# Kernel tuning notes

Measured on AMD Instinct MI355X. Metric: run time of the kernel, lower is better.

## Reference

```python
import jax, jax.numpy as jnp
import numpy as np

N = 50000      # nodes (== nbr_nodes)
E = 800000     # edges
D_IN = 128
D_H = 128
D_OUT = 47
NOISE_RATE = 0.1
EPS = 1e-12


def _lin_init(key, out_f, in_f):
    # rough Glorot-style init for a PyG Linear weight [out_f, in_f]
    s = 1.0 / np.sqrt(in_f)
    return jax.random.uniform(key, (out_f, in_f), jnp.float32, -s, s)


def setup_inputs() -> dict:
    key = jax.random.key(0)
    ks = jax.random.split(key, 13)
    inp = {
        "x": jax.random.normal(ks[0], (N, D_IN), jnp.float32),
        "edge_index": jax.random.randint(ks[1], (2, E), 0, N, dtype=jnp.int32),
        "noise": jax.random.normal(ks[2], (N, D_IN), jnp.float32),
        # layer 0: in -> hidden
        "W_l0": _lin_init(ks[3], D_H, D_IN),
        "b_l0": jnp.zeros((D_H,), jnp.float32),
        "W_r0": _lin_init(ks[4], D_H, D_IN),
        # layer 1: hidden -> hidden
        "W_l1": _lin_init(ks[5], D_H, D_H),
        "b_l1": jnp.zeros((D_H,), jnp.float32),
        "W_r1": _lin_init(ks[6], D_H, D_H),
        # layer 2: hidden -> out
        "W_l2": _lin_init(ks[7], D_OUT, D_H),
        "b_l2": jnp.zeros((D_OUT,), jnp.float32),
        "W_r2": _lin_init(ks[8], D_OUT, D_H),
    }
    return inp


def _sage_conv(x, src, dst, W_l, b_l, W_r):
    # PyG SAGEConv with mean aggregation:
    #   out_i = W_l @ mean_{j in N(i)} x_j + b_l + W_r @ x_i
    msg = x[src]                                              # [E, d] gather
    ssum = jax.ops.segment_sum(msg, dst, num_segments=N)      # [N, d]
    cnt = jax.ops.segment_sum(jnp.ones((src.shape[0], 1), x.dtype), dst,
                              num_segments=N)                 # [N, 1]
    agg = ssum / jnp.maximum(cnt, 1.0)                        # mean; 0 for isolated nodes
    return agg @ W_l.T + b_l + x @ W_r.T


def _branch(x, src, dst, params):
    # stacked SAGEConv; relu after all but last layer; dropout is identity (eval mode)
    h = None
    n_layers = len(params)
    for i, (W_l, b_l, W_r) in enumerate(params):
        x = _sage_conv(x, src, dst, W_l, b_l, W_r)
        if i != n_layers - 1:
            x = jax.nn.relu(x)
            h = x
    return h, jax.nn.log_softmax(x, axis=1), x


def _add_noise(x, noise):
    # n_id=None path: x + sign(x) * F.normalize(noise, dim=1) * noise_rate
    norm = jnp.sqrt(jnp.sum(noise * noise, axis=1, keepdims=True))
    unit = noise / jnp.maximum(norm, EPS)
    return x + jnp.sign(x) * unit * NOISE_RATE


def reference(x, edge_index, noise,
              W_l0, b_l0, W_r0, W_l1, b_l1, W_r1, W_l2, b_l2, W_r2):
    src, dst = edge_index[0], edge_index[1]
    params = [(W_l0, b_l0, W_r0), (W_l1, b_l1, W_r1), (W_l2, b_l2, W_r2)]
    h_p, y_p, z_p = _branch(x, src, dst, params)
    h_n, y_n, z_n = _branch(_add_noise(x, noise), src, dst, params)
    return (h_p, y_p, z_p, h_n, y_n, z_n)
```

## Files before the change

kernel.cpp:

```cpp
#include <hip/hip_runtime.h>
#include <math.h>


typedef unsigned int uint;
typedef unsigned short ushort;
typedef unsigned char uchar;
typedef short bf16x8 __attribute__((ext_vector_type(8)));
typedef float f32x4 __attribute__((ext_vector_type(4)));

__device__ __forceinline__ ushort f2b(float f) {
  union { float f; uint u; } v; v.f = f;
  uint u = v.u;
  return (ushort)((u + 0x7FFFu + ((u >> 16) & 1u)) >> 16);
}
__device__ __forceinline__ float b2f_lo(uint u) {
  union { uint u; float f; } v; v.u = u << 16; return v.f;
}
__device__ __forceinline__ float b2f_hi(uint u) {
  union { uint u; float f; } v; v.u = u & 0xFFFF0000u; return v.f;
}

#if __has_builtin(__builtin_amdgcn_cvt_f32_fp8)
__device__ __forceinline__ float dec8_0(uint u) { return __builtin_amdgcn_cvt_f32_fp8(u, 0); }
__device__ __forceinline__ float dec8_1(uint u) { return __builtin_amdgcn_cvt_f32_fp8(u, 1); }
__device__ __forceinline__ float dec8_2(uint u) { return __builtin_amdgcn_cvt_f32_fp8(u, 2); }
__device__ __forceinline__ float dec8_3(uint u) { return __builtin_amdgcn_cvt_f32_fp8(u, 3); }
#else
__device__ __forceinline__ float dec8_b(uint b) {
  uint s = (b >> 7) & 1u, ex = (b >> 3) & 0xFu, m = b & 7u;
  union { uint u; float f; } v;
  if (ex == 0) {
    v.f = (float)m * 0.001953125f;
    v.u |= s << 31;
    return v.f;
  }
  v.u = (s << 31) | ((ex + 120u) << 23) | (m << 20);
  return v.f;
}
__device__ __forceinline__ float dec8_0(uint u) { return dec8_b(u & 0xFFu); }
__device__ __forceinline__ float dec8_1(uint u) { return dec8_b((u >> 8) & 0xFFu); }
__device__ __forceinline__ float dec8_2(uint u) { return dec8_b((u >> 16) & 0xFFu); }
__device__ __forceinline__ float dec8_3(uint u) { return dec8_b((u >> 24) & 0xFFu); }
#endif

#if __has_builtin(__builtin_amdgcn_cvt_pk_fp8_f32)
__device__ __forceinline__ uchar enc8(float f) {
  return (uchar)(__builtin_amdgcn_cvt_pk_fp8_f32(f, f, 0u, false) & 0xFFu);
}
#else
__device__ __forceinline__ uchar enc8(float f) {
  union { float f; uint u; } v; v.f = f;
  uint s = v.u >> 31;
  uint a = v.u & 0x7FFFFFFFu;
  if (a >= 0x43E00000u) return (uchar)((s << 7) | 0x7Eu);
  if (a < 0x3C800000u) {
    float q = fabsf(f) * 512.0f;
    uint m = (uint)(q + 0.5f);
    return (uchar)((s << 7) | m);
  }
  uint r = a + 0x00080000u;
  if (r >= 0x43E00000u) return (uchar)((s << 7) | 0x7Eu);
  uint ex = (r >> 23) - 120u;
  uint m = (r >> 20) & 7u;
  return (uchar)((s << 7) | (ex << 3) | m);
}
#endif

__global__ __launch_bounds__(256) void count_kernel(
    const int* __restrict__ dst, int* __restrict__ cnt,
    int* __restrict__ rank, int E) {
  int e = blockIdx.x * blockDim.x + threadIdx.x;
  if (e >= E) return;
  rank[e] = atomicAdd(&cnt[dst[e]], 1);
}

__global__ __launch_bounds__(256) void scan_blocks(
    const int* __restrict__ cnt, int* __restrict__ loc,
    int* __restrict__ bsum, int n) {
  __shared__ int ls[4];
  int t = threadIdx.x;
  int base = blockIdx.x * 1024 + t * 4;
  int v[4];
  int s = 0;
#pragma unroll
  for (int i = 0; i < 4; ++i) {
    v[i] = (base + i < n) ? cnt[base + i] : 0;
    s += v[i];
  }
  int lane = t & 63, wid = t >> 6;
  int ps = s;
#pragma unroll
  for (int d = 1; d < 64; d <<= 1) {
    int o = __shfl_up(ps, d, 64);
    if (lane >= d) ps += o;
  }
  if (lane == 63) ls[wid] = ps;
  __syncthreads();
  if (t == 0) {
    int r = 0;
#pragma unroll
    for (int w = 0; w < 4; ++w) { int x = ls[w]; ls[w] = r; r += x; }
  }
  __syncthreads();
  int run = ps - s + ls[wid];
#pragma unroll
  for (int i = 0; i < 4; ++i) {
    if (base + i < n) loc[base + i] = run;
    run += v[i];
  }
  if (t == 255) bsum[blockIdx.x] = ps + ls[wid];
}

__global__ __launch_bounds__(256) void scan_bsums(int* __restrict__ bsum,
                                                  int nb) {
  __shared__ int ls[4];
  int t = threadIdx.x;
  int v = (t < nb) ? bsum[t] : 0;
  int lane = t & 63, wid = t >> 6;
  int ps = v;
#pragma unroll
  for (int d = 1; d < 64; d <<= 1) {
    int o = __shfl_up(ps, d, 64);
    if (lane >= d) ps += o;
  }
  if (lane == 63) ls[wid] = ps;
  __syncthreads();
  if (t == 0) {
    int r = 0;
#pragma unroll
    for (int w = 0; w < 4; ++w) { int x = ls[w]; ls[w] = r; r += x; }
  }
  __syncthreads();
  if (t < nb) bsum[t] = ps - v + ls[wid];
}

__global__ __launch_bounds__(256) void scan_apply(
    const int* __restrict__ loc, const int* __restrict__ bsum,
    int* __restrict__ off, int n, int E) {
  int i = blockIdx.x * 256 + threadIdx.x;
  if (i < n) off[i] = loc[i] + bsum[i >> 10];
  if (i == 0) off[n] = E;
}

__global__ __launch_bounds__(256) void fill_kernel(
    const int* __restrict__ src, const int* __restrict__ dst,
    const int* __restrict__ rank, const int* __restrict__ off,
    int* __restrict__ csr, int E) {
  int e = blockIdx.x * blockDim.x + threadIdx.x;
  if (e >= E) return;
  csr[off[dst[e]] + rank[e]] = src[e];
}

__global__ __launch_bounds__(256) void noisy_convert(
    const float* __restrict__ x, const float* __restrict__ noise,
    ushort* __restrict__ XB, int N) {
  int node = (blockIdx.x * blockDim.x + threadIdx.x) >> 6;
  int lane = threadIdx.x & 63;
  if (node >= N) return;
  size_t base = (size_t)node * 128 + 2 * lane;
  float2 nz = *(const float2*)(noise + base);
  float ss = nz.x * nz.x + nz.y * nz.y;
#pragma unroll
  for (int m = 1; m < 64; m <<= 1) ss += __shfl_xor(ss, m, 64);
  float scale = 0.1f / fmaxf(sqrtf(ss), 1e-12f);
  float2 xv = *(const float2*)(x + base);
  float s0 = (xv.x > 0.f) ? 1.f : ((xv.x < 0.f) ? -1.f : 0.f);
  float s1 = (xv.y > 0.f) ? 1.f : ((xv.y < 0.f) ? -1.f : 0.f);
  float n0 = xv.x + s0 * nz.x * scale;
  float n1 = xv.y + s1 * nz.y * scale;
  uint pc = ((uint)f2b(xv.y) << 16) | f2b(xv.x);
  uint pn = ((uint)f2b(n1) << 16) | f2b(n0);
  *(uint*)(XB + (size_t)(2 * node) * 128 + 2 * lane) = pc;
  *(uint*)(XB + (size_t)(2 * node + 1) * 128 + 2 * lane) = pn;
}

__global__ __launch_bounds__(256) void conv_weights(
    const float* __restrict__ Wl0, const float* __restrict__ Wr0,
    const float* __restrict__ Wl1, const float* __restrict__ Wr1,
    const float* __restrict__ Wl2, const float* __restrict__ Wr2,
    ushort* __restrict__ WB0, ushort* __restrict__ WB1,
    ushort* __restrict__ WB2) {
  int i = blockIdx.x * 256 + threadIdx.x;
  if (i < 16384) {
    WB0[i] = f2b(Wl0[i]);
    WB0[16384 + i] = f2b(Wr0[i]);
    WB1[i] = f2b(Wl1[i]);
    WB1[16384 + i] = f2b(Wr1[i]);
  }
  if (i < 6016) {
    WB2[i] = f2b(Wl2[i]);
    WB2[6016 + i] = f2b(Wr2[i]);
  }
}

__global__ __launch_bounds__(512) void gemm_fused(
    const ushort* __restrict__ A, const ushort* __restrict__ W,
    uchar* __restrict__ P8, float* __restrict__ Rf, int M) {
  __shared__ ushort As[128 * 72];
  __shared__ ushort Ws[256 * 72];
  int tid = threadIdx.x;
  int lane = tid & 63, wid = tid >> 6;
  int wm = wid & 1, wn = wid >> 1;
  int lrow = lane & 15, quad = lane >> 4;
  int row0 = blockIdx.x * 128;

  f32x4 acc[4][4];
#pragma unroll
  for (int mt = 0; mt < 4; ++mt)
#pragma unroll
    for (int nt = 0; nt < 4; ++nt) acc[mt][nt] = (f32x4)(0.f);

  for (int k0 = 0; k0 < 128; k0 += 64) {
    for (int c = tid; c < 128 * 8; c += 512) {
      int r = c >> 3, kc = c & 7;
      int gr = row0 + r;
      uint4 v = make_uint4(0, 0, 0, 0);
      if (gr < M) v = *(const uint4*)(A + (size_t)gr * 128 + k0 + kc * 8);
      *(uint4*)(As + r * 72 + kc * 8) = v;
    }
    for (int c = tid; c < 256 * 8; c += 512) {
      int r = c >> 3, kc = c & 7;
      uint4 v = *(const uint4*)(W + (size_t)r * 128 + k0 + kc * 8);
      *(uint4*)(Ws + r * 72 + kc * 8) = v;
    }
    __syncthreads();
#pragma unroll
    for (int ks = 0; ks < 64; ks += 32) {
      bf16x8 af[4], bw[4];
#pragma unroll
      for (int mt = 0; mt < 4; ++mt)
        af[mt] = *(const bf16x8*)(As + (wm * 64 + mt * 16 + lrow) * 72 + ks + quad * 8);
#pragma unroll
      for (int nt = 0; nt < 4; ++nt)
        bw[nt] = *(const bf16x8*)(Ws + (wn * 64 + nt * 16 + lrow) * 72 + ks + quad * 8);
#pragma unroll
      for (int mt = 0; mt < 4; ++mt)
#pragma unroll
        for (int nt = 0; nt < 4; ++nt)
          acc[mt][nt] = __builtin_amdgcn_mfma_f32_16x16x32_bf16(
              af[mt], bw[nt], acc[mt][nt], 0, 0, 0);
    }
    __syncthreads();
  }
  if (wn < 2) {
#pragma unroll
    for (int mt = 0; mt < 4; ++mt) {
#pragma unroll
      for (int nt = 0; nt < 4; ++nt) {
        int col = wn * 64 + nt * 16 + lrow;
#pragma unroll
        for (int rg = 0; rg < 4; rg += 2) {
          int row = row0 + wm * 64 + mt * 16 + quad * 4 + rg;
          if (row >= M) continue;
          int nd = row >> 1;
          float cv = acc[mt][nt][rg];
          float nv = acc[mt][nt][rg + 1];
          uchar c8 = enc8(cv);
          float cr = dec8_0((uint)c8);
          P8[(size_t)nd * 256 + col] = c8;
          P8[(size_t)nd * 256 + 128 + col] = enc8(nv - cr);
        }
      }
    }
  } else {
#pragma unroll
    for (int mt = 0; mt < 4; ++mt) {
#pragma unroll
      for (int nt = 0; nt < 4; ++nt) {
        int colR = (wn - 2) * 64 + nt * 16 + lrow;
#pragma unroll
        for (int rg = 0; rg < 4; ++rg) {
          int row = row0 + wm * 64 + mt * 16 + quad * 4 + rg;
          if (row >= M) continue;
          int nd = row >> 1, hf = row & 1;
          Rf[(size_t)nd * 256 + hf * 128 + colR] = acc[mt][nt][rg];
        }
      }
    }
  }
}

__global__ __launch_bounds__(256) void gemm_l2(
    const ushort* __restrict__ A, const ushort* __restrict__ W,
    ushort* __restrict__ Pzc, uchar* __restrict__ Pzd,
    float* __restrict__ Rz, int M) {
  constexpr int NT = 3;
  __shared__ ushort As[128 * 72];
  __shared__ ushort Ws[96 * 72];
  int tid = threadIdx.x;
  int lane = tid & 63, wid = tid >> 6;
  int wm = wid & 1, wn = wid >> 1;
  int lrow = lane & 15, quad = lane >> 4;
  int row0 = blockIdx.x * 128;

  f32x4 acc[4][NT];
#pragma unroll
  for (int mt = 0; mt < 4; ++mt)
#pragma unroll
    for (int nt = 0; nt < NT; ++nt) acc[mt][nt] = (f32x4)(0.f);

  for (int k0 = 0; k0 < 128; k0 += 64) {
    for (int c = tid; c < 128 * 8; c += 256) {
      int r = c >> 3, kc = c & 7;
      int gr = row0 + r;
      uint4 v = make_uint4(0, 0, 0, 0);
      if (gr < M) v = *(const uint4*)(A + (size_t)gr * 128 + k0 + kc * 8);
      *(uint4*)(As + r * 72 + kc * 8) = v;
    }
    for (int c = tid; c < 96 * 8; c += 256) {
      int r = c >> 3, kc = c & 7;
      uint4 v = make_uint4(0, 0, 0, 0);
      if (r < 94) v = *(const uint4*)(W + (size_t)r * 128 + k0 + kc * 8);
      *(uint4*)(Ws + r * 72 + kc * 8) = v;
    }
    __syncthreads();
#pragma unroll
    for (int ks = 0; ks < 64; ks += 32) {
      bf16x8 af[4], bw[NT];
#pragma unroll
      for (int mt = 0; mt < 4; ++mt)
        af[mt] = *(const bf16x8*)(As + (wm * 64 + mt * 16 + lrow) * 72 + ks + quad * 8);
#pragma unroll
      for (int nt = 0; nt < NT; ++nt)
        bw[nt] = *(const bf16x8*)(Ws + (wn * NT * 16 + nt * 16 + lrow) * 72 + ks + quad * 8);
#pragma unroll
      for (int mt = 0; mt < 4; ++mt)
#pragma unroll
        for (int nt = 0; nt < NT; ++nt)
          acc[mt][nt] = __builtin_amdgcn_mfma_f32_16x16x32_bf16(
              af[mt], bw[nt], acc[mt][nt], 0, 0, 0);
    }
    __syncthreads();
  }
#pragma unroll
  for (int mt = 0; mt < 4; ++mt) {
#pragma unroll
    for (int nt = 0; nt < NT; ++nt) {
      int col = wn * NT * 16 + nt * 16 + lrow;
#pragma unroll
      for (int rg = 0; rg < 4; rg += 2) {
        int row = row0 + wm * 64 + mt * 16 + quad * 4 + rg;
        if (row >= M) continue;
        int nd = row >> 1;
        float cv = acc[mt][nt][rg];
        float nv = acc[mt][nt][rg + 1];
        if (col < 47) {
          ushort cb = f2b(cv);
          Pzc[(size_t)nd * 64 + col] = cb;
          Pzd[(size_t)nd * 64 + col] = enc8(nv - b2f_lo((uint)cb));
        } else if (col < 94) {
          Rz[(size_t)nd * 128 + (col - 47)] = cv;
          Rz[(size_t)nd * 128 + 64 + (col - 47)] = nv;
        }
      }
    }
  }
}

template <bool WF32>
__global__ __launch_bounds__(256) void agg_dual128(
    const uchar* __restrict__ P8, const float* __restrict__ R2,
    const float* __restrict__ bias, const int* __restrict__ off,
    const int* __restrict__ csr, float* __restrict__ f0,
    float* __restrict__ f1, ushort* __restrict__ bout, int N) {
  int node = (blockIdx.x * blockDim.x + threadIdx.x) >> 6;
  int lane = threadIdx.x & 63;
  if (node >= N) return;
  int lq = lane & 31;
  int b = off[node], e = off[node + 1];
  float s0 = 0.f, s1 = 0.f, s2 = 0.f, s3 = 0.f;
  float t0 = 0.f, t1 = 0.f, t2 = 0.f, t3 = 0.f;
  int j = b;
  for (; j + 8 <= e; j += 8) {
    int a0 = csr[j],     a1 = csr[j + 1], a2 = csr[j + 2], a3 = csr[j + 3];
    int a4 = csr[j + 4], a5 = csr[j + 5], a6 = csr[j + 6], a7 = csr[j + 7];
    uint u0 = *(const uint*)(P8 + (size_t)a0 * 256 + 4 * lane);
    uint u1 = *(const uint*)(P8 + (size_t)a1 * 256 + 4 * lane);
    uint u2 = *(const uint*)(P8 + (size_t)a2 * 256 + 4 * lane);
    uint u3 = *(const uint*)(P8 + (size_t)a3 * 256 + 4 * lane);
    uint u4 = *(const uint*)(P8 + (size_t)a4 * 256 + 4 * lane);
    uint u5 = *(const uint*)(P8 + (size_t)a5 * 256 + 4 * lane);
    uint u6 = *(const uint*)(P8 + (size_t)a6 * 256 + 4 * lane);
    uint u7 = *(const uint*)(P8 + (size_t)a7 * 256 + 4 * lane);
    s0 += dec8_0(u0) + dec8_0(u1) + dec8_0(u2) + dec8_0(u3);
    s1 += dec8_1(u0) + dec8_1(u1) + dec8_1(u2) + dec8_1(u3);
    s2 += dec8_2(u0) + dec8_2(u1) + dec8_2(u2) + dec8_2(u3);
    s3 += dec8_3(u0) + dec8_3(u1) + dec8_3(u2) + dec8_3(u3);
    t0 += dec8_0(u4) + dec8_0(u5) + dec8_0(u6) + dec8_0(u7);
    t1 += dec8_1(u4) + dec8_1(u5) + dec8_1(u6) + dec8_1(u7);
    t2 += dec8_2(u4) + dec8_2(u5) + dec8_2(u6) + dec8_2(u7);
    t3 += dec8_3(u4) + dec8_3(u5) + dec8_3(u6) + dec8_3(u7);
  }
  if (j + 4 <= e) {
    int a0 = csr[j], a1 = csr[j + 1], a2 = csr[j + 2], a3 = csr[j + 3];
    uint u0 = *(const uint*)(P8 + (size_t)a0 * 256 + 4 * lane);
    uint u1 = *(const uint*)(P8 + (size_t)a1 * 256 + 4 * lane);
    uint u2 = *(const uint*)(P8 + (size_t)a2 * 256 + 4 * lane);
    uint u3 = *(const uint*)(P8 + (size_t)a3 * 256 + 4 * lane);
    s0 += dec8_0(u0) + dec8_0(u1) + dec8_0(u2) + dec8_0(u3);
    s1 += dec8_1(u0) + dec8_1(u1) + dec8_1(u2) + dec8_1(u3);
    s2 += dec8_2(u0) + dec8_2(u1) + dec8_2(u2) + dec8_2(u3);
    s3 += dec8_3(u0) + dec8_3(u1) + dec8_3(u2) + dec8_3(u3);
    j += 4;
  }
  for (; j < e; ++j) {
    uint u0 = *(const uint*)(P8 + (size_t)csr[j] * 256 + 4 * lane);
    s0 += dec8_0(u0);
    s1 += dec8_1(u0);
    s2 += dec8_2(u0);
    s3 += dec8_3(u0);
  }
  s0 += t0; s1 += t1; s2 += t2; s3 += t3;
  float o0 = __shfl_xor(s0, 32, 64);
  float o1 = __shfl_xor(s1, 32, 64);
  float o2 = __shfl_xor(s2, 32, 64);
  float o3 = __shfl_xor(s3, 32, 64);
  bool hi = lane >= 32;
  float m0 = hi ? (s0 + o0) : s0;
  float m1 = hi ? (s1 + o1) : s1;
  float m2 = hi ? (s2 + o2) : s2;
  float m3 = hi ? (s3 + o3) : s3;
  float invd = 1.f / (float)max(e - b, 1);
  float4 rv = *(const float4*)(R2 + (size_t)node * 256 + 4 * lane);
  float4 bb = *(const float4*)(bias + 4 * lq);
  float q0 = fmaxf(m0 * invd + bb.x + rv.x, 0.f);
  float q1 = fmaxf(m1 * invd + bb.y + rv.y, 0.f);
  float q2 = fmaxf(m2 * invd + bb.z + rv.z, 0.f);
  float q3 = fmaxf(m3 * invd + bb.w + rv.w, 0.f);
  size_t arow = (size_t)(2 * node + (hi ? 1 : 0)) * 128 + 4 * lq;
  ushort4 pk;
  pk.x = f2b(q0); pk.y = f2b(q1); pk.z = f2b(q2); pk.w = f2b(q3);
  *(ushort4*)(bout + arow) = pk;
  if (WF32) {
    float* dst = (hi ? f1 : f0) + (size_t)node * 128 + 4 * lq;
    *(float4*)dst = make_float4(q0, q1, q2, q3);
  }
}

__global__ __launch_bounds__(256) void agg47_dual(
    const ushort* __restrict__ Pzc, const uchar* __restrict__ Pzd,
    const float* __restrict__ Rz, const float* __restrict__ bias,
    const int* __restrict__ off, const int* __restrict__ csr,
    float* __restrict__ z0, float* __restrict__ z1, float* __restrict__ y0,
    float* __restrict__ y1, int N) {
  int node = (blockIdx.x * blockDim.x + threadIdx.x) >> 6;
  int lane = threadIdx.x & 63;
  if (node >= N) return;
  int lq = lane & 31;
  int b = off[node], e = off[node + 1];
  float a = 0.f, aa = 0.f;
  float g0 = 0.f, g1 = 0.f;
  float h0 = 0.f, h1 = 0.f;
  int j = b;
  for (; j + 8 <= e; j += 8) {
    int a0 = csr[j],     a1 = csr[j + 1], a2 = csr[j + 2], a3 = csr[j + 3];
    int a4 = csr[j + 4], a5 = csr[j + 5], a6 = csr[j + 6], a7 = csr[j + 7];
    uint c0 = Pzc[(size_t)a0 * 64 + lane];
    uint c1 = Pzc[(size_t)a1 * 64 + lane];
    uint c2 = Pzc[(size_t)a2 * 64 + lane];
    uint c3 = Pzc[(size_t)a3 * 64 + lane];
    uint c4 = Pzc[(size_t)a4 * 64 + lane];
    uint c5 = Pzc[(size_t)a5 * 64 + lane];
    uint c6 = Pzc[(size_t)a6 * 64 + lane];
    uint c7 = Pzc[(size_t)a7 * 64 + lane];
    uint d0 = *(const ushort*)(Pzd + (size_t)a0 * 64 + 2 * lq);
    uint d1 = *(const ushort*)(Pzd + (size_t)a1 * 64 + 2 * lq);
    uint d2 = *(const ushort*)(Pzd + (size_t)a2 * 64 + 2 * lq);
    uint d3 = *(const ushort*)(Pzd + (size_t)a3 * 64 + 2 * lq);
    uint d4 = *(const ushort*)(Pzd + (size_t)a4 * 64 + 2 * lq);
    uint d5 = *(const ushort*)(Pzd + (size_t)a5 * 64 + 2 * lq);
    uint d6 = *(const ushort*)(Pzd + (size_t)a6 * 64 + 2 * lq);
    uint d7 = *(const ushort*)(Pzd + (size_t)a7 * 64 + 2 * lq);
    a  += b2f_lo(c0) + b2f_lo(c1) + b2f_lo(c2) + b2f_lo(c3);
    aa += b2f_lo(c4) + b2f_lo(c5) + b2f_lo(c6) + b2f_lo(c7);
    g0 += dec8_0(d0) + dec8_0(d1) + dec8_0(d2) + dec8_0(d3);
    g1 += dec8_1(d0) + dec8_1(d1) + dec8_1(d2) + dec8_1(d3);
    h0 += dec8_0(d4) + dec8_0(d5) + dec8_0(d6) + dec8_0(d7);
    h1 += dec8_1(d4) + dec8_1(d5) + dec8_1(d6) + dec8_1(d7);
  }
  if (j + 4 <= e) {
    int a0 = csr[j], a1 = csr[j + 1], a2 = csr[j + 2], a3 = csr[j + 3];
    uint c0 = Pzc[(size_t)a0 * 64 + lane];
    uint c1 = Pzc[(size_t)a1 * 64 + lane];
    uint c2 = Pzc[(size_t)a2 * 64 + lane];
    uint c3 = Pzc[(size_t)a3 * 64 + lane];
    uint d0 = *(const ushort*)(Pzd + (size_t)a0 * 64 + 2 * lq);
    uint d1 = *(const ushort*)(Pzd + (size_t)a1 * 64 + 2 * lq);
    uint d2 = *(const ushort*)(Pzd + (size_t)a2 * 64 + 2 * lq);
    uint d3 = *(const ushort*)(Pzd + (size_t)a3 * 64 + 2 * lq);
    a  += b2f_lo(c0) + b2f_lo(c1) + b2f_lo(c2) + b2f_lo(c3);
    g0 += dec8_0(d0) + dec8_0(d1) + dec8_0(d2) + dec8_0(d3);
    g1 += dec8_1(d0) + dec8_1(d1) + dec8_1(d2) + dec8_1(d3);
    j += 4;
  }
  for (; j < e; ++j) {
    uint c0 = Pzc[(size_t)csr[j] * 64 + lane];
    uint d0 = *(const ushort*)(Pzd + (size_t)csr[j] * 64 + 2 * lq);
    a += b2f_lo(c0);
    g0 += dec8_0(d0);
    g1 += dec8_1(d0);
  }
  a += aa; g0 += h0; g1 += h1;
  float dd0 = __shfl(g0, lane >> 1, 64);
  float dd1 = __shfl(g1, lane >> 1, 64);
  float dl = (lane & 1) ? dd1 : dd0;
  bool v = lane < 47;
  float invd = 1.f / (float)max(e - b, 1);
  float rc = Rz[(size_t)node * 128 + lane];
  float rn = Rz[(size_t)node * 128 + 64 + lane];
  float bl = v ? bias[lane] : 0.f;
  float za = v ? (a * invd + bl + rc) : -INFINITY;
  float zn = v ? ((a + dl) * invd + bl + rn) : -INFINITY;
  float ma = za, mb = zn;
#pragma unroll
  for (int d = 1; d < 64; d <<= 1) {
    ma = fmaxf(ma, __shfl_xor(ma, d, 64));
    mb = fmaxf(mb, __shfl_xor(mb, d, 64));
  }
  float sa = v ? __expf(za - ma) : 0.f;
  float sb = v ? __expf(zn - mb) : 0.f;
#pragma unroll
  for (int d = 1; d < 64; d <<= 1) {
    sa += __shfl_xor(sa, d, 64);
    sb += __shfl_xor(sb, d, 64);
  }
  float lsa = logf(sa) + ma;
  float lsb = logf(sb) + mb;
  if (v) {
    z0[(size_t)node * 47 + lane] = za;
    y0[(size_t)node * 47 + lane] = za - lsa;
    z1[(size_t)node * 47 + lane] = zn;
    y1[(size_t)node * 47 + lane] = zn - lsb;
  }
}

extern "C" void kernel_launch(void* const* d_in, const int* in_sizes, int n_in,
                              void* d_out, int out_size, void* d_ws,
                              size_t ws_size, hipStream_t stream) {
  const float* x = (const float*)d_in[0];
  const int* ei = (const int*)d_in[1];
  const float* noise = (const float*)d_in[2];
  const float* Wl0 = (const float*)d_in[3];
  const float* bl0 = (const float*)d_in[4];
  const float* Wr0 = (const float*)d_in[5];
  const float* Wl1 = (const float*)d_in[6];
  const float* bl1 = (const float*)d_in[7];
  const float* Wr1 = (const float*)d_in[8];
  const float* Wl2 = (const float*)d_in[9];
  const float* bl2 = (const float*)d_in[10];
  const float* Wr2 = (const float*)d_in[11];

  const int N = in_sizes[0] / 128;
  const int E = in_sizes[1] / 2;
  const int M = 2 * N;

  float* out = (float*)d_out;
  float* h_p = out;
  float* y_p = h_p + (size_t)N * 128;
  float* z_p = y_p + (size_t)N * 47;
  float* h_n = z_p + (size_t)N * 47;
  float* y_n = h_n + (size_t)N * 128;
  float* z_n = y_n + (size_t)N * 47;

  char* w = (char*)d_ws;
  auto alloc = [&](size_t bytes) {
    void* p = (void*)w;
    w += (bytes + 511) & ~(size_t)511;
    return p;
  };
  ushort* XB = (ushort*)alloc((size_t)M * 128 * 2);
  uchar* P8 = (uchar*)alloc((size_t)N * 256);
  float* Rf = (float*)alloc((size_t)M * 128 * 4);
  ushort* WB0 = (ushort*)alloc(256 * 128 * 2);
  ushort* WB1 = (ushort*)alloc(256 * 128 * 2);
  ushort* WB2 = (ushort*)alloc(94 * 128 * 2);
  int* cnt = (int*)alloc((size_t)N * 4);
  int* off = (int*)alloc((size_t)(N + 1) * 4);
  int* rank = (int*)alloc((size_t)E * 4);
  int* loc = (int*)alloc((size_t)N * 4);
  int* bsum = (int*)alloc((size_t)256 * 4);
  int* csr = (int*)alloc((size_t)E * 4);
  ushort* Pzc = (ushort*)P8;
  uchar* Pzd = P8 + (size_t)N * 128;

  conv_weights<<<(16384 + 255) / 256, 256, 0, stream>>>(
      Wl0, Wr0, Wl1, Wr1, Wl2, Wr2, WB0, WB1, WB2);

  hipMemsetAsync(cnt, 0, (size_t)N * 4, stream);
  int eb = (E + 255) / 256;
  count_kernel<<<eb, 256, 0, stream>>>(ei + E, cnt, rank, E);
  int sb = (N + 1023) / 1024;
  scan_blocks<<<sb, 256, 0, stream>>>(cnt, loc, bsum, N);
  scan_bsums<<<1, 256, 0, stream>>>(bsum, sb);
  scan_apply<<<(N + 255) / 256, 256, 0, stream>>>(loc, bsum, off, N, E);
  fill_kernel<<<eb, 256, 0, stream>>>(ei, ei + E, rank, off, csr, E);

  int nwb = (N + 3) / 4;
  int rb = (M + 127) / 128;

  noisy_convert<<<nwb, 256, 0, stream>>>(x, noise, XB, N);

  gemm_fused<<<rb, 512, 0, stream>>>(XB, WB0, P8, Rf, M);
  agg_dual128<false><<<nwb, 256, 0, stream>>>(P8, Rf, bl0, off, csr, nullptr,
                                              nullptr, XB, N);
  gemm_fused<<<rb, 512, 0, stream>>>(XB, WB1, P8, Rf, M);
  agg_dual128<true><<<nwb, 256, 0, stream>>>(P8, Rf, bl1, off, csr, h_p, h_n,
                                             XB, N);
  gemm_l2<<<rb, 256, 0, stream>>>(XB, WB2, Pzc, Pzd, Rf, M);
  agg47_dual<<<nwb, 256, 0, stream>>>(Pzc, Pzd, Rf, bl2, off, csr, z_p, z_n,
                                      y_p, y_n, N);
}
```

Baseline: 415.9 us.

## Fuse prep kernels, store root term in bf16, add nontemporal loads/stores

Merges weight conversion, count zeroing and noisy-input conversion into one prep kernel, and folds the block-sum scan into scan_apply, which removes several launches and the memset. The per-node root projection written by the hidden-layer GEMM is now stored as bf16 instead of fp32, halving that intermediate's traffic at some precision cost. Nontemporal load/store builtins are applied across streaming accesses (CSR indices, outputs, intermediates) to reduce cache pollution. The layer-2 root term moves to its own fp32 buffer.

```diff
diff --git a/kernel.cpp b/kernel.cpp
--- a/kernel.cpp
+++ b/kernel.cpp
@@ -7,6 +7,18 @@
 typedef unsigned char uchar;
 typedef short bf16x8 __attribute__((ext_vector_type(8)));
 typedef float f32x4 __attribute__((ext_vector_type(4)));
+typedef float f32x2 __attribute__((ext_vector_type(2)));
+typedef uint u32x4 __attribute__((ext_vector_type(4)));
+typedef uint u32x2 __attribute__((ext_vector_type(2)));
+
+template <typename T>
+__device__ __forceinline__ T ldnt(const T* p) {
+  return __builtin_nontemporal_load(p);
+}
+template <typename T>
+__device__ __forceinline__ void stnt(T* p, T v) {
+  __builtin_nontemporal_store(v, p);
+}
 
 __device__ __forceinline__ ushort f2b(float f) {
   union { float f; uint u; } v; v.f = f;
@@ -66,12 +78,58 @@
 }
 #endif
 
+__global__ __launch_bounds__(256) void prep_kernel(
+    const float* __restrict__ x, const float* __restrict__ noise,
+    ushort* __restrict__ XB,
+    const float* __restrict__ Wl0, const float* __restrict__ Wr0,
+    const float* __restrict__ Wl1, const float* __restrict__ Wr1,
+    const float* __restrict__ Wl2, const float* __restrict__ Wr2,
+    ushort* __restrict__ WB0, ushort* __restrict__ WB1,
+    ushort* __restrict__ WB2, int* __restrict__ cnt, int N) {
+  int blk = blockIdx.x, t = threadIdx.x;
+  if (blk < 64) {
+    int i = blk * 256 + t;
+    WB0[i] = f2b(Wl0[i]);
+    WB0[16384 + i] = f2b(Wr0[i]);
+    WB1[i] = f2b(Wl1[i]);
+    WB1[16384 + i] = f2b(Wr1[i]);
+    if (i < 6016) {
+      WB2[i] = f2b(Wl2[i]);
+      WB2[6016 + i] = f2b(Wr2[i]);
+    }
+  }
+  {
+    int i = blk * 256 + t;
+    if (i < N) cnt[i] = 0;
+  }
+  int node = (blk * 256 + t) >> 6;
+  int lane = t & 63;
+  if (node >= N) return;
+  size_t base = (size_t)node * 128 + 2 * lane;
+  f32x2 nz = ldnt((const f32x2*)(noise + base));
+  float ss = nz.x * nz.x + nz.y * nz.y;
+#pragma unroll
+  for (int m = 1; m < 64; m <<= 1) ss += __shfl_xor(ss, m, 64);
+  float scale = 0.1f / fmaxf(sqrtf(ss), 1e-12f);
+  f32x2 xv = ldnt((const f32x2*)(x + base));
+  float s0 = (xv.x > 0.f) ? 1.f : ((xv.x < 0.f) ? -1.f : 0.f);
+  float s1 = (xv.y > 0.f) ? 1.f : ((xv.y < 0.f) ? -1.f : 0.f);
+  float n0 = xv.x + s0 * nz.x * scale;
+  float n1 = xv.y + s1 * nz.y * scale;
+  uint pc = ((uint)f2b(xv.y) << 16) | f2b(xv.x);
+  uint pn = ((uint)f2b(n1) << 16) | f2b(n0);
+  stnt((uint*)(XB + (size_t)(2 * node) * 128 + 2 * lane), pc);
+  stnt((uint*)(XB + (size_t)(2 * node + 1) * 128 + 2 * lane), pn);
+}
+
 __global__ __launch_bounds__(256) void count_kernel(
     const int* __restrict__ dst, int* __restrict__ cnt,
     int* __restrict__ rank, int E) {
   int e = blockIdx.x * blockDim.x + threadIdx.x;
   if (e >= E) return;
-  rank[e] = atomicAdd(&cnt[dst[e]], 1);
+  int d = ldnt(dst + e);
+  int r = atomicAdd(&cnt[d], 1);
+  stnt(rank + e, r);
 }
 
 __global__ __launch_bounds__(256) void scan_blocks(
@@ -111,9 +169,11 @@
   if (t == 255) bsum[blockIdx.x] = ps + ls[wid];
 }
 
-__global__ __launch_bounds__(256) void scan_bsums(int* __restrict__ bsum,
-                                                  int nb) {
+__global__ __launch_bounds__(256) void scan_apply(
+    const int* __restrict__ loc, const int* __restrict__ bsum,
+    int* __restrict__ off, int n, int E, int nb) {
   __shared__ int ls[4];
+  __shared__ int ex[256];
   int t = threadIdx.x;
   int v = (t < nb) ? bsum[t] : 0;
   int lane = t & 63, wid = t >> 6;
@@ -131,14 +191,10 @@
     for (int w = 0; w < 4; ++w) { int x = ls[w]; ls[w] = r; r += x; }
   }
   __syncthreads();
-  if (t < nb) bsum[t] = ps - v + ls[wid];
-}
-
-__global__ __launch_bounds__(256) void scan_apply(
-    const int* __restrict__ loc, const int* __restrict__ bsum,
-    int* __restrict__ off, int n, int E) {
-  int i = blockIdx.x * 256 + threadIdx.x;
-  if (i < n) off[i] = loc[i] + bsum[i >> 10];
+  ex[t] = ps - v + ls[wid];
+  __syncthreads();
+  int i = blockIdx.x * 256 + t;
+  if (i < n) off[i] = loc[i] + ex[i >> 10];
   if (i == 0) off[n] = E;
 }
 
@@ -148,54 +204,15 @@
     int* __restrict__ csr, int E) {
   int e = blockIdx.x * blockDim.x + threadIdx.x;
   if (e >= E) return;
-  csr[off[dst[e]] + rank[e]] = src[e];
-}
-
-__global__ __launch_bounds__(256) void noisy_convert(
-    const float* __restrict__ x, const float* __restrict__ noise,
-    ushort* __restrict__ XB, int N) {
-  int node = (blockIdx.x * blockDim.x + threadIdx.x) >> 6;
-  int lane = threadIdx.x & 63;
-  if (node >= N) return;
-  size_t base = (size_t)node * 128 + 2 * lane;
-  float2 nz = *(const float2*)(noise + base);
-  float ss = nz.x * nz.x + nz.y * nz.y;
-#pragma unroll
-  for (int m = 1; m < 64; m <<= 1) ss += __shfl_xor(ss, m, 64);
-  float scale = 0.1f / fmaxf(sqrtf(ss), 1e-12f);
-  float2 xv = *(const float2*)(x + base);
-  float s0 = (xv.x > 0.f) ? 1.f : ((xv.x < 0.f) ? -1.f : 0.f);
-  float s1 = (xv.y > 0.f) ? 1.f : ((xv.y < 0.f) ? -1.f : 0.f);
-  float n0 = xv.x + s0 * nz.x * scale;
-  float n1 = xv.y + s1 * nz.y * scale;
-  uint pc = ((uint)f2b(xv.y) << 16) | f2b(xv.x);
-  uint pn = ((uint)f2b(n1) << 16) | f2b(n0);
-  *(uint*)(XB + (size_t)(2 * node) * 128 + 2 * lane) = pc;
-  *(uint*)(XB + (size_t)(2 * node + 1) * 128 + 2 * lane) = pn;
-}
-
-__global__ __launch_bounds__(256) void conv_weights(
-    const float* __restrict__ Wl0, const float* __restrict__ Wr0,
-    const float* __restrict__ Wl1, const float* __restrict__ Wr1,
-    const float* __restrict__ Wl2, const float* __restrict__ Wr2,
-    ushort* __restrict__ WB0, ushort* __restrict__ WB1,
-    ushort* __restrict__ WB2) {
-  int i = blockIdx.x * 256 + threadIdx.x;
-  if (i < 16384) {
-    WB0[i] = f2b(Wl0[i]);
-    WB0[16384 + i] = f2b(Wr0[i]);
-    WB1[i] = f2b(Wl1[i]);
-    WB1[16384 + i] = f2b(Wr1[i]);
-  }
-  if (i < 6016) {
-    WB2[i] = f2b(Wl2[i]);
-    WB2[6016 + i] = f2b(Wr2[i]);
-  }
+  int d = ldnt(dst + e);
+  int s = ldnt(src + e);
+  int r = ldnt(rank + e);
+  stnt(csr + off[d] + r, s);
 }
 
 __global__ __launch_bounds__(512) void gemm_fused(
     const ushort* __restrict__ A, const ushort* __restrict__ W,
-    uchar* __restrict__ P8, float* __restrict__ Rf, int M) {
+    uchar* __restrict__ P8, ushort* __restrict__ Rb, int M) {
   __shared__ ushort As[128 * 72];
   __shared__ ushort Ws[256 * 72];
   int tid = threadIdx.x;
@@ -214,14 +231,14 @@
     for (int c = tid; c < 128 * 8; c += 512) {
       int r = c >> 3, kc = c & 7;
       int gr = row0 + r;
-      uint4 v = make_uint4(0, 0, 0, 0);
-      if (gr < M) v = *(const uint4*)(A + (size_t)gr * 128 + k0 + kc * 8);
-      *(uint4*)(As + r * 72 + kc * 8) = v;
+      u32x4 v = (u32x4)(0u);
+      if (gr < M) v = ldnt((const u32x4*)(A + (size_t)gr * 128 + k0 + kc * 8));
+      *(u32x4*)(As + r * 72 + kc * 8) = v;
     }
     for (int c = tid; c < 256 * 8; c += 512) {
       int r = c >> 3, kc = c & 7;
-      uint4 v = *(const uint4*)(W + (size_t)r * 128 + k0 + kc * 8);
-      *(uint4*)(Ws + r * 72 + kc * 8) = v;
+      u32x4 v = *(const u32x4*)(W + (size_t)r * 128 + k0 + kc * 8);
+      *(u32x4*)(Ws + r * 72 + kc * 8) = v;
     }
     __syncthreads();
 #pragma unroll
@@ -257,8 +274,8 @@
           float nv = acc[mt][nt][rg + 1];
           uchar c8 = enc8(cv);
           float cr = dec8_0((uint)c8);
-          P8[(size_t)nd * 256 + col] = c8;
-          P8[(size_t)nd * 256 + 128 + col] = enc8(nv - cr);
+          stnt(P8 + (size_t)nd * 256 + col, c8);
+          stnt(P8 + (size_t)nd * 256 + 128 + col, enc8(nv - cr));
         }
       }
     }
@@ -273,7 +290,7 @@
           int row = row0 + wm * 64 + mt * 16 + quad * 4 + rg;
           if (row >= M) continue;
           int nd = row >> 1, hf = row & 1;
-          Rf[(size_t)nd * 256 + hf * 128 + colR] = acc[mt][nt][rg];
+          stnt(Rb + (size_t)nd * 256 + hf * 128 + colR, f2b(acc[mt][nt][rg]));
         }
       }
     }
@@ -303,15 +320,15 @@
     for (int c = tid; c < 128 * 8; c += 256) {
       int r = c >> 3, kc = c & 7;
       int gr = row0 + r;
-      uint4 v = make_uint4(0, 0, 0, 0);
-      if (gr < M) v = *(const uint4*)(A + (size_t)gr * 128 + k0 + kc * 8);
-      *(uint4*)(As + r * 72 + kc * 8) = v;
+      u32x4 v = (u32x4)(0u);
+      if (gr < M) v = ldnt((const u32x4*)(A + (size_t)gr * 128 + k0 + kc * 8));
+      *(u32x4*)(As + r * 72 + kc * 8) = v;
     }
     for (int c = tid; c < 96 * 8; c += 256) {
       int r = c >> 3, kc = c & 7;
-      uint4 v = make_uint4(0, 0, 0, 0);
-      if (r < 94) v = *(const uint4*)(W + (size_t)r * 128 + k0 + kc * 8);
-      *(uint4*)(Ws + r * 72 + kc * 8) = v;
+      u32x4 v = (u32x4)(0u);
+      if (r < 94) v = *(const u32x4*)(W + (size_t)r * 128 + k0 + kc * 8);
+      *(u32x4*)(Ws + r * 72 + kc * 8) = v;
     }
     __syncthreads();
 #pragma unroll
@@ -346,11 +363,11 @@
         float nv = acc[mt][nt][rg + 1];
         if (col < 47) {
           ushort cb = f2b(cv);
-          Pzc[(size_t)nd * 64 + col] = cb;
-          Pzd[(size_t)nd * 64 + col] = enc8(nv - b2f_lo((uint)cb));
+          stnt(Pzc + (size_t)nd * 64 + col, cb);
+          stnt(Pzd + (size_t)nd * 64 + col, enc8(nv - b2f_lo((uint)cb)));
         } else if (col < 94) {
-          Rz[(size_t)nd * 128 + (col - 47)] = cv;
-          Rz[(size_t)nd * 128 + 64 + (col - 47)] = nv;
+          stnt(Rz + (size_t)nd * 128 + (col - 47), cv);
+          stnt(Rz + (size_t)nd * 128 + 64 + (col - 47), nv);
         }
       }
     }
@@ -359,7 +376,7 @@
 
 template <bool WF32>
 __global__ __launch_bounds__(256) void agg_dual128(
-    const uchar* __restrict__ P8, const float* __restrict__ R2,
+    const uchar* __restrict__ P8, const ushort* __restrict__ Rb,
     const float* __restrict__ bias, const int* __restrict__ off,
     const int* __restrict__ csr, float* __restrict__ f0,
     float* __restrict__ f1, ushort* __restrict__ bout, int N) {
@@ -372,8 +389,10 @@
   float t0 = 0.f, t1 = 0.f, t2 = 0.f, t3 = 0.f;
   int j = b;
   for (; j + 8 <= e; j += 8) {
-    int a0 = csr[j],     a1 = csr[j + 1], a2 = csr[j + 2], a3 = csr[j + 3];
-    int a4 = csr[j + 4], a5 = csr[j + 5], a6 = csr[j + 6], a7 = csr[j + 7];
+    int a0 = ldnt(csr + j),     a1 = ldnt(csr + j + 1);
+    int a2 = ldnt(csr + j + 2), a3 = ldnt(csr + j + 3);
+    int a4 = ldnt(csr + j + 4), a5 = ldnt(csr + j + 5);
+    int a6 = ldnt(csr + j + 6), a7 = ldnt(csr + j + 7);
     uint u0 = *(const uint*)(P8 + (size_t)a0 * 256 + 4 * lane);
     uint u1 = *(const uint*)(P8 + (size_t)a1 * 256 + 4 * lane);
     uint u2 = *(const uint*)(P8 + (size_t)a2 * 256 + 4 * lane);
@@ -392,7 +411,8 @@
     t3 += dec8_3(u4) + dec8_3(u5) + dec8_3(u6) + dec8_3(u7);
   }
   if (j + 4 <= e) {
-    int a0 = csr[j], a1 = csr[j + 1], a2 = csr[j + 2], a3 = csr[j + 3];
+    int a0 = ldnt(csr + j),     a1 = ldnt(csr + j + 1);
+    int a2 = ldnt(csr + j + 2), a3 = ldnt(csr + j + 3);
     uint u0 = *(const uint*)(P8 + (size_t)a0 * 256 + 4 * lane);
     uint u1 = *(const uint*)(P8 + (size_t)a1 * 256 + 4 * lane);
     uint u2 = *(const uint*)(P8 + (size_t)a2 * 256 + 4 * lane);
@@ -404,7 +424,7 @@
     j += 4;
   }
   for (; j < e; ++j) {
-    uint u0 = *(const uint*)(P8 + (size_t)csr[j] * 256 + 4 * lane);
+    uint u0 = *(const uint*)(P8 + (size_t)ldnt(csr + j) * 256 + 4 * lane);
     s0 += dec8_0(u0);
     s1 += dec8_1(u0);
     s2 += dec8_2(u0);
@@ -421,19 +441,23 @@
   float m2 = hi ? (s2 + o2) : s2;
   float m3 = hi ? (s3 + o3) : s3;
   float invd = 1.f / (float)max(e - b, 1);
-  float4 rv = *(const float4*)(R2 + (size_t)node * 256 + 4 * lane);
+  u32x2 rp = ldnt((const u32x2*)(Rb + (size_t)node * 256 + 4 * lane));
+  float rvx = b2f_lo(rp.x), rvy = b2f_hi(rp.x);
+  float rvz = b2f_lo(rp.y), rvw = b2f_hi(rp.y);
   float4 bb = *(const float4*)(bias + 4 * lq);
-  float q0 = fmaxf(m0 * invd + bb.x + rv.x, 0.f);
-  float q1 = fmaxf(m1 * invd + bb.y + rv.y, 0.f);
-  float q2 = fmaxf(m2 * invd + bb.z + rv.z, 0.f);
-  float q3 = fmaxf(m3 * invd + bb.w + rv.w, 0.f);
+  float q0 = fmaxf(m0 * invd + bb.x + rvx, 0.f);
+  float q1 = fmaxf(m1 * invd + bb.y + rvy, 0.f);
+  float q2 = fmaxf(m2 * invd + bb.z + rvz, 0.f);
+  float q3 = fmaxf(m3 * invd + bb.w + rvw, 0.f);
   size_t arow = (size_t)(2 * node + (hi ? 1 : 0)) * 128 + 4 * lq;
-  ushort4 pk;
-  pk.x = f2b(q0); pk.y = f2b(q1); pk.z = f2b(q2); pk.w = f2b(q3);
-  *(ushort4*)(bout + arow) = pk;
+  u32x2 pk;
+  pk.x = ((uint)f2b(q1) << 16) | f2b(q0);
+  pk.y = ((uint)f2b(q3) << 16) | f2b(q2);
+  stnt((u32x2*)(bout + arow), pk);
   if (WF32) {
     float* dst = (hi ? f1 : f0) + (size_t)node * 128 + 4 * lq;
-    *(float4*)dst = make_float4(q0, q1, q2, q3);
+    f32x4 qv; qv.x = q0; qv.y = q1; qv.z = q2; qv.w = q3;
+    stnt((f32x4*)dst, qv);
   }
 }
 
@@ -453,8 +477,10 @@
   float h0 = 0.f, h1 = 0.f;
   int j = b;
   for (; j + 8 <= e; j += 8) {
-    int a0 = csr[j],     a1 = csr[j + 1], a2 = csr[j + 2], a3 = csr[j + 3];
-    int a4 = csr[j + 4], a5 = csr[j + 5], a6 = csr[j + 6], a7 = csr[j + 7];
+    int a0 = ldnt(csr + j),     a1 = ldnt(csr + j + 1);
+    int a2 = ldnt(csr + j + 2), a3 = ldnt(csr + j + 3);
+    int a4 = ldnt(csr + j + 4), a5 = ldnt(csr + j + 5);
+    int a6 = ldnt(csr + j + 6), a7 = ldnt(csr + j + 7);
     uint c0 = Pzc[(size_t)a0 * 64 + lane];
     uint c1 = Pzc[(size_t)a1 * 64 + lane];
     uint c2 = Pzc[(size_t)a2 * 64 + lane];
@@ -479,7 +505,8 @@
     h1 += dec8_1(d4) + dec8_1(d5) + dec8_1(d6) + dec8_1(d7);
   }
   if (j + 4 <= e) {
-    int a0 = csr[j], a1 = csr[j + 1], a2 = csr[j + 2], a3 = csr[j + 3];
+    int a0 = ldnt(csr + j),     a1 = ldnt(csr + j + 1);
+    int a2 = ldnt(csr + j + 2), a3 = ldnt(csr + j + 3);
     uint c0 = Pzc[(size_t)a0 * 64 + lane];
     uint c1 = Pzc[(size_t)a1 * 64 + lane];
     uint c2 = Pzc[(size_t)a2 * 64 + lane];
@@ -494,8 +521,9 @@
     j += 4;
   }
   for (; j < e; ++j) {
-    uint c0 = Pzc[(size_t)csr[j] * 64 + lane];
-    uint d0 = *(const ushort*)(Pzd + (size_t)csr[j] * 64 + 2 * lq);
+    int a0 = ldnt(csr + j);
+    uint c0 = Pzc[(size_t)a0 * 64 + lane];
+    uint d0 = *(const ushort*)(Pzd + (size_t)a0 * 64 + 2 * lq);
     a += b2f_lo(c0);
     g0 += dec8_0(d0);
     g1 += dec8_1(d0);
@@ -506,8 +534,8 @@
   float dl = (lane & 1) ? dd1 : dd0;
   bool v = lane < 47;
   float invd = 1.f / (float)max(e - b, 1);
-  float rc = Rz[(size_t)node * 128 + lane];
-  float rn = Rz[(size_t)node * 128 + 64 + lane];
+  float rc = ldnt(Rz + (size_t)node * 128 + lane);
+  float rn = ldnt(Rz + (size_t)node * 128 + 64 + lane);
   float bl = v ? bias[lane] : 0.f;
   float za = v ? (a * invd + bl + rc) : -INFINITY;
   float zn = v ? ((a + dl) * invd + bl + rn) : -INFINITY;
@@ -527,10 +555,10 @@
   float lsa = logf(sa) + ma;
   float lsb = logf(sb) + mb;
   if (v) {
-    z0[(size_t)node * 47 + lane] = za;
-    y0[(size_t)node * 47 + lane] = za - lsa;
-    z1[(size_t)node * 47 + lane] = zn;
-    y1[(size_t)node * 47 + lane] = zn - lsb;
+    stnt(z0 + (size_t)node * 47 + lane, za);
+    stnt(y0 + (size_t)node * 47 + lane, za - lsa);
+    stnt(z1 + (size_t)node * 47 + lane, zn);
+    stnt(y1 + (size_t)node * 47 + lane, zn - lsb);
   }
 }
 
@@ -570,7 +598,8 @@
   };
   ushort* XB = (ushort*)alloc((size_t)M * 128 * 2);
   uchar* P8 = (uchar*)alloc((size_t)N * 256);
-  float* Rf = (float*)alloc((size_t)M * 128 * 4);
+  ushort* Rb = (ushort*)alloc((size_t)M * 128 * 2);
+  float* Rz = (float*)alloc((size_t)N * 128 * 4);
   ushort* WB0 = (ushort*)alloc(256 * 128 * 2);
   ushort* WB1 = (ushort*)alloc(256 * 128 * 2);
   ushort* WB2 = (ushort*)alloc(94 * 128 * 2);
@@ -583,30 +612,26 @@
   ushort* Pzc = (ushort*)P8;
   uchar* Pzd = P8 + (size_t)N * 128;
 
-  conv_weights<<<(16384 + 255) / 256, 256, 0, stream>>>(
-      Wl0, Wr0, Wl1, Wr1, Wl2, Wr2, WB0, WB1, WB2);
-
-  hipMemsetAsync(cnt, 0, (size_t)N * 4, stream);
-  int eb = (E + 255) / 256;
-  count_kernel<<<eb, 256, 0, stream>>>(ei + E, cnt, rank, E);
-  int sb = (N + 1023) / 1024;
-  scan_blocks<<<sb, 256, 0, stream>>>(cnt, loc, bsum, N);
-  scan_bsums<<<1, 256, 0, stream>>>(bsum, sb);
-  scan_apply<<<(N + 255) / 256, 256, 0, stream>>>(loc, bsum, off, N, E);
-  fill_kernel<<<eb, 256, 0, stream>>>(ei, ei + E, rank, off, csr, E);
-
   int nwb = (N + 3) / 4;
   int rb = (M + 127) / 128;
-
-  noisy_convert<<<nwb, 256, 0, stream>>>(x, noise, XB, N);
-
-  gemm_fused<<<rb, 512, 0, stream>>>(XB, WB0, P8, Rf, M);
-  agg_dual128<false><<<nwb, 256, 0, stream>>>(P8, Rf, bl0, off, csr, nullptr,
+  int eb = (E + 255) / 256;
+  int sb = (N + 1023) / 1024;
+
+  prep_kernel<<<nwb, 256, 0, stream>>>(x, noise, XB, Wl0, Wr0, Wl1, Wr1, Wl2,
+                                       Wr2, WB0, WB1, WB2, cnt, N);
+
+  count_kernel<<<eb, 256, 0, stream>>>(ei + E, cnt, rank, E);
+  scan_blocks<<<sb, 256, 0, stream>>>(cnt, loc, bsum, N);
+  scan_apply<<<(N + 255) / 256, 256, 0, stream>>>(loc, bsum, off, N, E, sb);
+  fill_kernel<<<eb, 256, 0, stream>>>(ei, ei + E, rank, off, csr, E);
+
+  gemm_fused<<<rb, 512, 0, stream>>>(XB, WB0, P8, Rb, M);
+  agg_dual128<false><<<nwb, 256, 0, stream>>>(P8, Rb, bl0, off, csr, nullptr,
                                               nullptr, XB, N);
-  gemm_fused<<<rb, 512, 0, stream>>>(XB, WB1, P8, Rf, M);
-  agg_dual128<true><<<nwb, 256, 0, stream>>>(P8, Rf, bl1, off, csr, h_p, h_n,
+  gemm_fused<<<rb, 512, 0, stream>>>(XB, WB1, P8, Rb, M);
+  agg_dual128<true><<<nwb, 256, 0, stream>>>(P8, Rb, bl1, off, csr, h_p, h_n,
                                              XB, N);
-  gemm_l2<<<rb, 256, 0, stream>>>(XB, WB2, Pzc, Pzd, Rf, M);
-  agg47_dual<<<nwb, 256, 0, stream>>>(Pzc, Pzd, Rf, bl2, off, csr, z_p, z_n,
+  gemm_l2<<<rb, 256, 0, stream>>>(XB, WB2, Pzc, Pzd, Rz, M);
+  agg47_dual<<<nwb, 256, 0, stream>>>(Pzc, Pzd, Rz, bl2, off, csr, z_p, z_n,
                                       y_p, y_n, N);
 }
```

Measured after the change: 499.0 us. 20.0% more time.
